# Performance work log

Measured on AMD Instinct MI355X. Metric: run time of the kernel, lower is better.

## Reference

```python
import jax, jax.numpy as jnp
import numpy as np

D_H, D_G, D_PROJ = 1280, 768, 256
SCALE = D_PROJ ** (-0.5)

def setup_inputs() -> dict:
    key = jax.random.key(0)
    k1, k2, k3, k4 = jax.random.split(key, 4)
    B, L, T = 8, 4096, 512
    H = jax.random.normal(k1, (B, L, D_H), dtype=jnp.float32)
    G = jax.random.normal(k2, (B, T, D_G), dtype=jnp.float32)
    attn_mask = jnp.zeros((B, L), dtype=bool)  # True = pad/ignore
    # nn.Linear weights: (out_features, in_features)
    Wk = jax.random.normal(k3, (D_PROJ, D_H), dtype=jnp.float32) * (D_H ** -0.5)
    Wq = jax.random.normal(k4, (D_PROJ, D_G), dtype=jnp.float32) * (D_G ** -0.5)
    return {"H": H, "G": G, "attn_mask": attn_mask, "Wk": Wk, "Wq": Wq}

def reference(H, G, attn_mask, Wk, Wq):
    # K = Wk(H): (B,L,P); Q = Wq(G): (B,T,P)
    K = jnp.einsum('bld,pd->blp', H, Wk)
    Q = jnp.einsum('btd,pd->btp', G, Wq)
    # scores (B,T,L); streaming two-pass softmax in the original is exactly
    # softmax over L -> compute it stably in one fused expression here.
    logits = jnp.einsum('btp,blp->btl', Q, K) * SCALE
    logits = jnp.where(attn_mask[:, None, :], -jnp.inf, logits)
    alpha = jax.nn.softmax(logits, axis=-1)
    Z = jnp.einsum('btl,bld->btd', alpha, H)  # (B,T,Dh)
    return Z
```

## Files before the change

kernel.cpp:

```cpp
#include <hip/hip_runtime.h>
#include <hip/hip_bf16.h>
#include <stdint.h>


typedef float f32x4 __attribute__((ext_vector_type(4)));
typedef short bf16x8 __attribute__((ext_vector_type(8)));

__device__ __forceinline__ unsigned short f2bf(float f) {
    __hip_bfloat16 h = __float2bfloat16(f);
    return __builtin_bit_cast(unsigned short, h);
}
__device__ __forceinline__ float bf2f(unsigned short h) {
    union { uint32_t u; float f; } v; v.u = ((uint32_t)h) << 16;
    return v.f;
}

__device__ __forceinline__ int xcdswz(int bx, int nbx) {
    int cpx = nbx >> 3;
    return (bx & 7) * cpx + (bx >> 3);
}

__device__ __forceinline__ void gload16(const unsigned short* g, unsigned short* l) {
    __builtin_amdgcn_global_load_lds(
        (const __attribute__((address_space(1))) void*)g,
        (__attribute__((address_space(3))) void*)l,
        16, 0, 0);
}

__device__ __forceinline__ int lidx(int row, int kshort) {
    return row * 40 + (((kshort >> 3) ^ ((row >> 3) & 3)) << 3) + (kshort & 7);
}

template<bool WRITE_HBT>
__global__ __launch_bounds__(256)
void gemm_proj(const float* __restrict__ Ap, const float* __restrict__ Bp,
               unsigned short* __restrict__ Cp, int M, int N, int K,
               unsigned short* __restrict__ Hbt)
{
    __shared__ __align__(16) unsigned short lA[128 * 40];
    __shared__ __align__(16) unsigned short lB[128 * 40];

    const int bx = xcdswz(blockIdx.x, gridDim.x);
    const int nt = N >> 7;
    const int tm = bx / nt;
    const int tn = bx % nt;
    const int tid = threadIdx.x;
    const int lane = tid & 63, wv = tid >> 6;
    const int wr = wv >> 1, wc = wv & 1;
    const int fr = lane & 15, fk = lane >> 4;

    f32x4 acc[4][4] = {};

    for (int k0 = 0; k0 < K; k0 += 32) {
        {
            const float* A = Ap + (long)tm * 128 * K + k0;
            #pragma unroll
            for (int it = 0; it < 4; ++it) {
                int chunk = it * 256 + tid;
                int row = chunk >> 3;
                int kc  = (chunk & 7) << 2;
                const float4 v = *(const float4*)(A + (long)row * K + kc);
                ushort4 w;
                w.x = f2bf(v.x); w.y = f2bf(v.y); w.z = f2bf(v.z); w.w = f2bf(v.w);
                *(ushort4*)(&lA[lidx(row, kc)]) = w;
                if constexpr (WRITE_HBT) {
                    if (tn == 0) {
                        int gm = tm * 128 + row;
                        int bb = gm >> 12, ll = gm & 4095;
                        unsigned short wa[4] = { w.x, w.y, w.z, w.w };
                        #pragma unroll
                        for (int j = 0; j < 4; ++j)
                            Hbt[((long)bb * 1280 + k0 + kc + j) * 4096 + ll] = wa[j];
                    }
                }
            }
        }
        {
            const float* B = Bp + (long)tn * 128 * K + k0;
            #pragma unroll
            for (int it = 0; it < 4; ++it) {
                int chunk = it * 256 + tid;
                int row = chunk >> 3;
                int kc  = (chunk & 7) << 2;
                const float4 v = *(const float4*)(B + (long)row * K + kc);
                ushort4 w;
                w.x = f2bf(v.x); w.y = f2bf(v.y); w.z = f2bf(v.z); w.w = f2bf(v.w);
                *(ushort4*)(&lB[lidx(row, kc)]) = w;
            }
        }
        __syncthreads();
        bf16x8 af[4], bfr[4];
        #pragma unroll
        for (int i = 0; i < 4; ++i)
            af[i] = *(const bf16x8*)(&lA[lidx(wr * 64 + i * 16 + fr, fk * 8)]);
        #pragma unroll
        for (int i = 0; i < 4; ++i)
            bfr[i] = *(const bf16x8*)(&lB[lidx(wc * 64 + i * 16 + fr, fk * 8)]);
        #pragma unroll
        for (int mi = 0; mi < 4; ++mi)
            #pragma unroll
            for (int ni = 0; ni < 4; ++ni)
                acc[mi][ni] = __builtin_amdgcn_mfma_f32_16x16x32_bf16(af[mi], bfr[ni], acc[mi][ni], 0, 0, 0);
        __syncthreads();
    }

    unsigned short* C = Cp + ((long)tm * 128) * N + (long)tn * 128;
    #pragma unroll
    for (int mi = 0; mi < 4; ++mi)
        #pragma unroll
        for (int ni = 0; ni < 4; ++ni)
            #pragma unroll
            for (int j = 0; j < 4; ++j) {
                int m = wr * 64 + mi * 16 + fk * 4 + j;
                int n = wc * 64 + ni * 16 + fr;
                C[(long)m * N + n] = f2bf(acc[mi][ni][j]);
            }
}

template<bool OF32>
__global__ __launch_bounds__(256)
void gemm_bt16s(const unsigned short* __restrict__ Ap, const unsigned short* __restrict__ Bp,
                void* __restrict__ Cp, int M, int N, int K,
                long sA, long sB, long sC, float scale)
{
    __shared__ __align__(16) unsigned short lA[128 * 64];
    __shared__ __align__(16) unsigned short lB[128 * 64];

    const int bx = xcdswz(blockIdx.x, gridDim.x);
    const int nt = N >> 7;
    const int tm = bx / nt, tn = bx % nt;
    const int b  = blockIdx.y;
    const int tid = threadIdx.x;
    const int lane = tid & 63, wv = tid >> 6;
    const int wr = wv >> 1, wc = wv & 1;
    const int fr = lane & 15, fk = lane >> 4;

    f32x4 acc[4][4] = {};

    const unsigned short* A0 = Ap + (long)b * sA + (long)tm * 128 * K;
    const unsigned short* B0 = Bp + (long)b * sB + (long)tn * 128 * K;

    for (int k0 = 0; k0 < K; k0 += 64) {
        #pragma unroll
        for (int q = 0; q < 4; ++q) {
            int slot = wv * 256 + q * 64 + lane;
            int row = slot >> 3, c = slot & 7;
            int ks = (c ^ (row & 7)) << 3;
            gload16(A0 + (long)row * K + k0 + ks, lA + (size_t)(wv * 256 + q * 64) * 8);
            gload16(B0 + (long)row * K + k0 + ks, lB + (size_t)(wv * 256 + q * 64) * 8);
        }
        __syncthreads();
        bf16x8 af[2][4], bfv[2][4];
        #pragma unroll
        for (int ks = 0; ks < 2; ++ks) {
            int csw = ((ks * 4 + fk) ^ (fr & 7)) << 3;
            #pragma unroll
            for (int i = 0; i < 4; ++i) {
                af[ks][i]  = *(const bf16x8*)(lA + (wr * 64 + i * 16 + fr) * 64 + csw);
                bfv[ks][i] = *(const bf16x8*)(lB + (wc * 64 + i * 16 + fr) * 64 + csw);
            }
        }
        #pragma unroll
        for (int mi = 0; mi < 4; ++mi)
            #pragma unroll
            for (int ni = 0; ni < 4; ++ni)
                #pragma unroll
                for (int ks = 0; ks < 2; ++ks)
                    acc[mi][ni] = __builtin_amdgcn_mfma_f32_16x16x32_bf16(af[ks][mi], bfv[ks][ni], acc[mi][ni], 0, 0, 0);
        __syncthreads();
    }

    if constexpr (OF32) {
        float* C = (float*)Cp + (long)b * sC + ((long)tm * 128) * N + (long)tn * 128;
        #pragma unroll
        for (int mi = 0; mi < 4; ++mi)
            #pragma unroll
            for (int ni = 0; ni < 4; ++ni)
                #pragma unroll
                for (int j = 0; j < 4; ++j) {
                    int m = wr * 64 + mi * 16 + fk * 4 + j;
                    int n = wc * 64 + ni * 16 + fr;
                    C[(long)m * N + n] = acc[mi][ni][j] * scale;
                }
    } else {
        unsigned short* C = (unsigned short*)Cp + (long)b * sC + ((long)tm * 128) * N + (long)tn * 128;
        #pragma unroll
        for (int mi = 0; mi < 4; ++mi)
            #pragma unroll
            for (int ni = 0; ni < 4; ++ni)
                #pragma unroll
                for (int j = 0; j < 4; ++j) {
                    int m = wr * 64 + mi * 16 + fk * 4 + j;
                    int n = wc * 64 + ni * 16 + fr;
                    C[(long)m * N + n] = f2bf(acc[mi][ni][j] * scale);
                }
    }
}

__global__ __launch_bounds__(256)
void gemm_kn(const unsigned short* __restrict__ Ap, const float* __restrict__ Bp,
             float* __restrict__ Cp, int M, int N, int K,
             long sA, long sB, long sC)
{
    __shared__ __align__(16) unsigned short lA[128 * 40];
    __shared__ __align__(16) unsigned short lB[64 * 40];

    const int bx = xcdswz(blockIdx.x, gridDim.x);
    const int mt = M >> 7;
    const int tm = bx % mt;
    const int tn = bx / mt;
    const int b  = blockIdx.y;
    const int tid = threadIdx.x;
    const int lane = tid & 63, wv = tid >> 6;
    const int wr = wv >> 1, wc = wv & 1;
    const int fr = lane & 15, fk = lane >> 4;

    f32x4 acc[4][2] = {};

    const unsigned short* A0 = Ap + (long)b * sA + (long)tm * 128 * K;
    const int nn    = tid & 63;
    const int khalf = tid >> 6;

    for (int k0 = 0; k0 < K; k0 += 32) {
        #pragma unroll
        for (int it = 0; it < 2; ++it) {
            int chunk = it * 256 + tid;
            int row = chunk >> 2;
            int kc  = (chunk & 3) << 3;
            *(uint4*)(&lA[lidx(row, kc)]) = *(const uint4*)(A0 + (long)row * K + k0 + kc);
        }
        {
            const float* Bb = Bp + (long)b * sB + (long)(k0 + khalf * 8) * N + (long)tn * 64 + nn;
            unsigned short t8[8];
            #pragma unroll
            for (int kk = 0; kk < 8; ++kk)
                t8[kk] = f2bf(Bb[(long)kk * N]);
            *(uint4*)(&lB[lidx(nn, khalf * 8)]) = *(uint4*)(&t8[0]);
        }
        __syncthreads();
        bf16x8 af[4], bfr[2];
        #pragma unroll
        for (int i = 0; i < 4; ++i)
            af[i] = *(const bf16x8*)(&lA[lidx(wr * 64 + i * 16 + fr, fk * 8)]);
        #pragma unroll
        for (int i = 0; i < 2; ++i)
            bfr[i] = *(const bf16x8*)(&lB[lidx(wc * 32 + i * 16 + fr, fk * 8)]);
        #pragma unroll
        for (int mi = 0; mi < 4; ++mi)
            #pragma unroll
            for (int ni = 0; ni < 2; ++ni)
                acc[mi][ni] = __builtin_amdgcn_mfma_f32_16x16x32_bf16(af[mi], bfr[ni], acc[mi][ni], 0, 0, 0);
        __syncthreads();
    }

    float* C = Cp + (long)b * sC + ((long)tm * 128) * N + (long)tn * 64;
    #pragma unroll
    for (int mi = 0; mi < 4; ++mi)
        #pragma unroll
        for (int ni = 0; ni < 2; ++ni)
            #pragma unroll
            for (int j = 0; j < 4; ++j) {
                int m = wr * 64 + mi * 16 + fk * 4 + j;
                int n = wc * 32 + ni * 16 + fr;
                C[(long)m * N + n] = acc[mi][ni][j];
            }
}

__global__ __launch_bounds__(256)
void softmax_rows(unsigned short* __restrict__ S, const unsigned char* __restrict__ mask)
{
    const int row = blockIdx.x;
    const int b = row >> 9;
    const long base = (long)row * 4096;
    const int tid = threadIdx.x, lane = tid & 63, wv = tid >> 6;
    __shared__ float red[8];

    uint4 s0 = *(const uint4*)(S + base + tid * 16);
    uint4 s1 = *(const uint4*)(S + base + tid * 16 + 8);
    uint4 mv = *(const uint4*)(mask + (long)b * 4096 + tid * 16);
    const unsigned char* mb = (const unsigned char*)&mv;

    unsigned int words[8] = { s0.x, s0.y, s0.z, s0.w, s1.x, s1.y, s1.z, s1.w };
    float x[16];
    #pragma unroll
    for (int i = 0; i < 8; ++i) {
        x[2 * i]     = bf2f((unsigned short)(words[i] & 0xffffu));
        x[2 * i + 1] = bf2f((unsigned short)(words[i] >> 16));
    }
    #pragma unroll
    for (int i = 0; i < 16; ++i)
        if (mb[i]) x[i] = -1e30f;

    float m = x[0];
    #pragma unroll
    for (int i = 1; i < 16; ++i) m = fmaxf(m, x[i]);
    #pragma unroll
    for (int off = 32; off; off >>= 1) m = fmaxf(m, __shfl_xor(m, off));
    if (lane == 0) red[wv] = m;
    __syncthreads();
    m = fmaxf(fmaxf(red[0], red[1]), fmaxf(red[2], red[3]));

    float p[16];
    float s = 0.f;
    #pragma unroll
    for (int i = 0; i < 16; ++i) { p[i] = __expf(x[i] - m); s += p[i]; }
    #pragma unroll
    for (int off = 32; off; off >>= 1) s += __shfl_xor(s, off);
    if (lane == 0) red[4 + wv] = s;
    __syncthreads();
    s = (red[4] + red[5]) + (red[6] + red[7]);
    const float inv = 1.0f / s;

    unsigned int ow[8];
    #pragma unroll
    for (int i = 0; i < 8; ++i) {
        unsigned int lo = f2bf(p[2 * i] * inv);
        unsigned int hi = f2bf(p[2 * i + 1] * inv);
        ow[i] = lo | (hi << 16);
    }
    uint4 o0 = { ow[0], ow[1], ow[2], ow[3] };
    uint4 o1 = { ow[4], ow[5], ow[6], ow[7] };
    *(uint4*)(S + base + tid * 16)     = o0;
    *(uint4*)(S + base + tid * 16 + 8) = o1;
}

extern "C" void kernel_launch(void* const* d_in, const int* in_sizes, int n_in,
                              void* d_out, int out_size, void* d_ws, size_t ws_size,
                              hipStream_t stream)
{
    const float*         H    = (const float*)d_in[0];
    const float*         G    = (const float*)d_in[1];
    const unsigned char* mask = (const unsigned char*)d_in[2];
    const float*         Wk   = (const float*)d_in[3];
    const float*         Wq   = (const float*)d_in[4];
    float*               out  = (float*)d_out;

    const long nK = (long)8 * 4096 * 256;
    const long nQ = (long)8 * 512 * 256;
    const long nS = (long)8 * 512 * 4096;
    const long nH = (long)8 * 1280 * 4096;

    unsigned short* Kb  = (unsigned short*)d_ws;
    unsigned short* Qb  = Kb + nK;
    unsigned short* Sb  = Qb + nQ;
    unsigned short* Hbt = Sb + nS;
    const bool big = ws_size >= (size_t)(nK + nQ + nS + nH) * 2;

    if (big) {
        gemm_proj<true><<<dim3(512, 1), 256, 0, stream>>>(
            H, Wk, Kb, 32768, 256, 1280, Hbt);
        gemm_proj<false><<<dim3(64, 1), 256, 0, stream>>>(
            G, Wq, Qb, 4096, 256, 768, nullptr);
        gemm_bt16s<false><<<dim3(128, 8), 256, 0, stream>>>(
            Qb, Kb, Sb, 512, 4096, 256,
            (long)512 * 256, (long)4096 * 256, (long)512 * 4096, 0.0625f);
        softmax_rows<<<dim3(4096), 256, 0, stream>>>(Sb, mask);
        gemm_bt16s<true><<<dim3(40, 8), 256, 0, stream>>>(
            Sb, Hbt, out, 512, 1280, 4096,
            (long)512 * 4096, (long)1280 * 4096, (long)512 * 1280, 1.0f);
    } else {
        gemm_proj<false><<<dim3(512, 1), 256, 0, stream>>>(
            H, Wk, Kb, 32768, 256, 1280, nullptr);
        gemm_proj<false><<<dim3(64, 1), 256, 0, stream>>>(
            G, Wq, Qb, 4096, 256, 768, nullptr);
        gemm_bt16s<false><<<dim3(128, 8), 256, 0, stream>>>(
            Qb, Kb, Sb, 512, 4096, 256,
            (long)512 * 256, (long)4096 * 256, (long)512 * 4096, 0.0625f);
        softmax_rows<<<dim3(4096), 256, 0, stream>>>(Sb, mask);
        gemm_kn<<<dim3(80, 8), 256, 0, stream>>>(
            Sb, H, out, 512, 1280, 4096,
            (long)512 * 4096, (long)4096 * 1280, (long)512 * 1280);
    }
}
```

Before: 282.3 us.

## Pre-convert H to bf16 with coalesced LDS transpose, run K projection as bf16 GEMM

Adds a dedicated H conversion kernel that writes both row-major bf16 H and a transposed bf16 copy through a swizzled LDS tile, so the transpose stores are coalesced. The old path did scattered 2-byte strided stores inside the projection GEMM. Wk is also converted to bf16, and the K projection now uses the bf16 gemm_bt16s path instead of converting fp32 inside the GEMM. This costs an extra bf16 copy of H in workspace plus two extra launches. If the workspace is too small, the code falls back to the older paths.

Result: faster. 271.7 us (-3.8%).

```diff
diff --git a/kernel.cpp b/kernel.cpp
--- a/kernel.cpp
+++ b/kernel.cpp
@@ -31,11 +31,65 @@
     return row * 40 + (((kshort >> 3) ^ ((row >> 3) & 3)) << 3) + (kshort & 7);
 }
 
-template<bool WRITE_HBT>
+__global__ __launch_bounds__(256)
+void cvt_f32_bf16(const float* __restrict__ in, unsigned short* __restrict__ out, long n4)
+{
+    long i = (long)blockIdx.x * 256 + threadIdx.x;
+    if (i >= n4) return;
+    float4 v = ((const float4*)in)[i];
+    ushort4 w;
+    w.x = f2bf(v.x); w.y = f2bf(v.y); w.z = f2bf(v.z); w.w = f2bf(v.w);
+    ((ushort4*)out)[i] = w;
+}
+
+template<bool WRITE_HB>
+__global__ __launch_bounds__(256)
+void cvt_h(const float* __restrict__ H, unsigned short* __restrict__ Hbt,
+           unsigned short* __restrict__ Hb)
+{
+    __shared__ unsigned short lT[64 * 72];
+    const int ntile = 64 * 20 * 8;
+    for (int tileid = blockIdx.x; tileid < ntile; tileid += gridDim.x) {
+        int tmp = tileid;
+        const int dt = tmp % 20; tmp /= 20;
+        const int lt = tmp % 64;
+        const int b  = tmp / 64;
+        const int l0 = lt * 64, d0 = dt * 64;
+        const float* Hs = H + ((long)b * 4096 + l0) * 1280 + d0;
+        #pragma unroll
+        for (int it = 0; it < 4; ++it) {
+            int chunk = it * 256 + threadIdx.x;
+            int lr = chunk >> 4, dc4 = (chunk & 15) << 2;
+            float4 v = *(const float4*)(Hs + (long)lr * 1280 + dc4);
+            unsigned short w[4] = { f2bf(v.x), f2bf(v.y), f2bf(v.z), f2bf(v.w) };
+            if constexpr (WRITE_HB) {
+                ushort4 wb = { w[0], w[1], w[2], w[3] };
+                *(ushort4*)(Hb + ((long)b * 4096 + l0 + lr) * 1280 + d0 + dc4) = wb;
+            }
+            #pragma unroll
+            for (int j = 0; j < 4; ++j) {
+                int d = dc4 + j;
+                int sl = (lr & 15) | ((((lr >> 4) ^ (d >> 2)) & 3) << 4);
+                lT[d * 72 + sl] = w[j];
+            }
+        }
+        __syncthreads();
+        {
+            int drow = threadIdx.x >> 2, lc = threadIdx.x & 3;
+            int slc = lc ^ ((drow >> 2) & 3);
+            const uint4* src = (const uint4*)(lT + drow * 72 + slc * 16);
+            unsigned short* dst = Hbt + ((long)b * 1280 + d0 + drow) * 4096 + l0 + lc * 16;
+            uint4 v0 = src[0], v1 = src[1];
+            *(uint4*)(dst)     = v0;
+            *(uint4*)(dst + 8) = v1;
+        }
+        __syncthreads();
+    }
+}
+
 __global__ __launch_bounds__(256)
 void gemm_proj(const float* __restrict__ Ap, const float* __restrict__ Bp,
-               unsigned short* __restrict__ Cp, int M, int N, int K,
-               unsigned short* __restrict__ Hbt)
+               unsigned short* __restrict__ Cp, int M, int N, int K)
 {
     __shared__ __align__(16) unsigned short lA[128 * 40];
     __shared__ __align__(16) unsigned short lB[128 * 40];
@@ -63,16 +117,6 @@
                 ushort4 w;
                 w.x = f2bf(v.x); w.y = f2bf(v.y); w.z = f2bf(v.z); w.w = f2bf(v.w);
                 *(ushort4*)(&lA[lidx(row, kc)]) = w;
-                if constexpr (WRITE_HBT) {
-                    if (tn == 0) {
-                        int gm = tm * 128 + row;
-                        int bb = gm >> 12, ll = gm & 4095;
-                        unsigned short wa[4] = { w.x, w.y, w.z, w.w };
-                        #pragma unroll
-                        for (int j = 0; j < 4; ++j)
-                            Hbt[((long)bb * 1280 + k0 + kc + j) * 4096 + ll] = wa[j];
-                    }
-                }
             }
         }
         {
@@ -339,18 +383,35 @@
     const long nQ = (long)8 * 512 * 256;
     const long nS = (long)8 * 512 * 4096;
     const long nH = (long)8 * 1280 * 4096;
+    const long nW = (long)256 * 1280;
 
     unsigned short* Kb  = (unsigned short*)d_ws;
     unsigned short* Qb  = Kb + nK;
     unsigned short* Sb  = Qb + nQ;
     unsigned short* Hbt = Sb + nS;
-    const bool big = ws_size >= (size_t)(nK + nQ + nS + nH) * 2;
-
-    if (big) {
-        gemm_proj<true><<<dim3(512, 1), 256, 0, stream>>>(
-            H, Wk, Kb, 32768, 256, 1280, Hbt);
-        gemm_proj<false><<<dim3(64, 1), 256, 0, stream>>>(
-            G, Wq, Qb, 4096, 256, 768, nullptr);
+    unsigned short* Hb  = Hbt + nH;
+    unsigned short* Wkb = Hb + nH;
+
+    const size_t need2 = (size_t)(nK + nQ + nS + nH + nH + nW) * 2;
+    const size_t need1 = (size_t)(nK + nQ + nS + nH) * 2;
+
+    if (ws_size >= need2) {
+        cvt_f32_bf16<<<dim3(320), 256, 0, stream>>>(Wk, Wkb, nW / 4);
+        cvt_h<true><<<dim3(2048), 256, 0, stream>>>(H, Hbt, Hb);
+        gemm_bt16s<false><<<dim3(512, 1), 256, 0, stream>>>(
+            Hb, Wkb, Kb, 32768, 256, 1280, 0, 0, 0, 1.0f);
+        gemm_proj<<<dim3(64, 1), 256, 0, stream>>>(G, Wq, Qb, 4096, 256, 768);
+        gemm_bt16s<false><<<dim3(128, 8), 256, 0, stream>>>(
+            Qb, Kb, Sb, 512, 4096, 256,
+            (long)512 * 256, (long)4096 * 256, (long)512 * 4096, 0.0625f);
+        softmax_rows<<<dim3(4096), 256, 0, stream>>>(Sb, mask);
+        gemm_bt16s<true><<<dim3(40, 8), 256, 0, stream>>>(
+            Sb, Hbt, out, 512, 1280, 4096,
+            (long)512 * 4096, (long)1280 * 4096, (long)512 * 1280, 1.0f);
+    } else if (ws_size >= need1) {
+        gemm_proj<<<dim3(512, 1), 256, 0, stream>>>(H, Wk, Kb, 32768, 256, 1280);
+        gemm_proj<<<dim3(64, 1), 256, 0, stream>>>(G, Wq, Qb, 4096, 256, 768);
+        cvt_h<false><<<dim3(2048), 256, 0, stream>>>(H, Hbt, nullptr);
         gemm_bt16s<false><<<dim3(128, 8), 256, 0, stream>>>(
             Qb, Kb, Sb, 512, 4096, 256,
             (long)512 * 256, (long)4096 * 256, (long)512 * 4096, 0.0625f);
@@ -359,10 +420,8 @@
             Sb, Hbt, out, 512, 1280, 4096,
             (long)512 * 4096, (long)1280 * 4096, (long)512 * 1280, 1.0f);
     } else {
-        gemm_proj<false><<<dim3(512, 1), 256, 0, stream>>>(
-            H, Wk, Kb, 32768, 256, 1280, nullptr);
-        gemm_proj<false><<<dim3(64, 1), 256, 0, stream>>>(
-            G, Wq, Qb, 4096, 256, 768, nullptr);
+        gemm_proj<<<dim3(512, 1), 256, 0, stream>>>(H, Wk, Kb, 32768, 256, 1280);
+        gemm_proj<<<dim3(64, 1), 256, 0, stream>>>(G, Wq, Qb, 4096, 256, 768);
         gemm_bt16s<false><<<dim3(128, 8), 256, 0, stream>>>(
             Qb, Kb, Sb, 512, 4096, 256,
             (long)512 * 256, (long)4096 * 256, (long)512 * 4096, 0.0625f);
```
